# Kernel tuning notes

Measured on AMD Instinct MI355X. Metric: run time of the kernel, lower is better.

The kernel has to match this reference:

```python
import jax, jax.numpy as jnp
import numpy as np

SEQ_LEN = 12      # PRED_LEN
H_DIM = 128
EMB_DIM = 64
NPEDS = 65536


def setup_inputs() -> dict:
    key = jax.random.key(0)
    ks = jax.random.split(key, 12)
    s = 0.05
    return {
        "last_pos": jax.random.normal(ks[0], (NPEDS, 2), jnp.float32),
        "last_pos_rel": jax.random.normal(ks[1], (NPEDS, 2), jnp.float32),
        "h0": jax.random.normal(ks[2], (NPEDS, H_DIM), jnp.float32),
        "c0": jax.random.normal(ks[3], (NPEDS, H_DIM), jnp.float32),
        # LSTM params (torch gate order: i, f, g, o)
        "w_ih": jax.random.normal(ks[4], (4 * H_DIM, EMB_DIM), jnp.float32) * s,
        "w_hh": jax.random.normal(ks[5], (4 * H_DIM, H_DIM), jnp.float32) * s,
        "b_ih": jax.random.normal(ks[6], (4 * H_DIM,), jnp.float32) * s,
        "b_hh": jax.random.normal(ks[7], (4 * H_DIM,), jnp.float32) * s,
        # spatial_embedding: Linear(2, EMB_DIM)
        "w_se": jax.random.normal(ks[8], (EMB_DIM, 2), jnp.float32) * s,
        "b_se": jax.random.normal(ks[9], (EMB_DIM,), jnp.float32) * s,
        # hidden2pos: Linear(H_DIM, 2)
        "w_hp": jax.random.normal(ks[10], (2, H_DIM), jnp.float32) * s,
        "b_hp": jax.random.normal(ks[11], (2,), jnp.float32) * s,
    }


def reference(last_pos, last_pos_rel, h0, c0,
              w_ih, w_hh, b_ih, b_hh, w_se, b_se, w_hp, b_hp):
    b = b_ih + b_hh  # fold the two LSTM biases
    dec_in0 = last_pos_rel @ w_se.T + b_se          # [N, EMB]

    def step(carry, _):
        h, c, dec_in, lp = carry
        gates = dec_in @ w_ih.T + h @ w_hh.T + b    # [N, 4H]
        i, f, g, o = jnp.split(gates, 4, axis=-1)
        c = jax.nn.sigmoid(f) * c + jax.nn.sigmoid(i) * jnp.tanh(g)
        h = jax.nn.sigmoid(o) * jnp.tanh(c)
        rel = h @ w_hp.T + b_hp                     # [N, 2]
        lp = rel + lp                               # curr_pos
        dec_in = rel @ w_se.T + b_se                # next embedding input
        return (h, c, dec_in, lp), rel

    _, rels = jax.lax.scan(step, (h0, c0, dec_in0, last_pos), None, length=SEQ_LEN)
    return rels  # [SEQ_LEN, N, 2] == pred_traj_fake_rel
```

## Files before the change

### kernel.cpp

```cpp
#include <hip/hip_runtime.h>
#include <hip/hip_bf16.h>

typedef __attribute__((ext_vector_type(8))) short bf16x8;
typedef __attribute__((ext_vector_type(4))) short bf16x4;
typedef __attribute__((ext_vector_type(4))) float f32x4;
typedef __attribute__((ext_vector_type(2))) float f32x2;

#define NPEDS 65536
#define SEQ 12
#define HD 128
#define ED 64
#define MBLK 128
#define NPT 8
#define WHH_FRAGS 128
#define WEFF_FRAGS 132
#define NFRAGS (WHH_FRAGS + WEFF_FRAGS)
#define L2E 1.44269504088896340736f
#define NEG2L (-2.88539008177792681472f)

__device__ __forceinline__ short f2bf(float x) {
  __hip_bfloat16 b = __float2bfloat16(x);
  return __builtin_bit_cast(short, b);
}
__device__ __forceinline__ float exp2_(float x) {
#if __has_builtin(__builtin_amdgcn_exp2f)
  return __builtin_amdgcn_exp2f(x);
#else
  return exp2f(x);
#endif
}

__device__ __forceinline__ int hoff(int Pt, int cg, int lhi, int llo) {
  return (((Pt * 8 + cg) * 4 + lhi) * 16 + llo) * 4;
}

__global__ void prep_kernel(const float* __restrict__ w_ih,
                            const float* __restrict__ w_hh,
                            const float* __restrict__ w_se,
                            const float* __restrict__ w_hp,
                            const float* __restrict__ b_ih,
                            const float* __restrict__ b_hh,
                            const float* __restrict__ b_se,
                            const float* __restrict__ b_hp,
                            short* __restrict__ wsB, float* __restrict__ fl) {
  int t = blockIdx.x * 256 + threadIdx.x;
  if (t < WHH_FRAGS * 64) {
    int frag = t >> 6, l = t & 63;
    int cc = frag >> 4, g = (frag >> 2) & 3, kt = frag & 3;
    float fac = (g == 2) ? 2.0f * L2E : L2E;
    int n = g * HD + cc * 16 + (l & 15);
    bf16x8 v;
#pragma unroll
    for (int e = 0; e < 8; ++e) {
      int k = kt * 32 + ((l >> 4) << 2) + (e & 3) + ((e >> 2) << 4);
      v[e] = f2bf(w_hh[n * HD + k] * fac);
    }
    *(bf16x8*)(wsB + (size_t)frag * 512 + l * 8) = v;
  } else if (t < NFRAGS * 64) {
    int u = t - WHH_FRAGS * 64;
    int frag = u >> 6, l = u & 63;
    int llo = l & 15;
    int ks[8];
#pragma unroll
    for (int e = 0; e < 8; ++e)
      ks[e] = (frag & 3) * 32 + ((l >> 4) << 2) + (e & 3) + ((e >> 2) << 4);
    float acc[8];
    if (frag < 128) {
      int cc = frag >> 4, g = (frag >> 2) & 3;
      float fac = (g == 2) ? 2.0f * L2E : L2E;
      int n = g * HD + cc * 16 + llo;
#pragma unroll
      for (int e = 0; e < 8; ++e) acc[e] = w_hh[n * HD + ks[e]];
      for (int j = 0; j < ED; ++j) {
        float wij = w_ih[n * ED + j];
        float se0 = w_se[2 * j], se1 = w_se[2 * j + 1];
#pragma unroll
        for (int e = 0; e < 8; ++e)
          acc[e] += wij * (se0 * w_hp[ks[e]] + se1 * w_hp[HD + ks[e]]);
      }
#pragma unroll
      for (int e = 0; e < 8; ++e) acc[e] *= fac;
    } else {
#pragma unroll
      for (int e = 0; e < 8; ++e)
        acc[e] = (llo < 2) ? w_hp[llo * HD + ks[e]] : 0.f;
    }
    bf16x8 v;
#pragma unroll
    for (int e = 0; e < 8; ++e) v[e] = f2bf(acc[e]);
    *(bf16x8*)(wsB + (size_t)(WHH_FRAGS + frag) * 512 + l * 8) = v;
  } else if (t < NFRAGS * 64 + 512) {
    int n = t - NFRAGS * 64;
    float fac = ((n >> 7) == 2) ? 2.0f * L2E : L2E;
    float b = b_ih[n] + b_hh[n];
    float s0 = 0.f, w20 = 0.f, w21 = 0.f;
    for (int j = 0; j < ED; ++j) {
      float wij = w_ih[n * ED + j];
      s0 += wij * b_se[j];
      w20 += wij * w_se[2 * j];
      w21 += wij * w_se[2 * j + 1];
    }
    fl[n] = fac * (b + s0 + w20 * b_hp[0] + w21 * b_hp[1]);
    fl[512 + n] = fac * (b + s0);
    fl[1024 + 2 * n] = fac * w20;
    fl[1024 + 2 * n + 1] = fac * w21;
  }
}

__global__ __launch_bounds__(512, 2) void lstm_kernel(
    const float* __restrict__ lpr, const float* __restrict__ h0,
    const float* __restrict__ c0, const float* __restrict__ b_hp,
    const short* __restrict__ wsB, const float* __restrict__ fl,
    float* __restrict__ out) {
  __shared__ short hb[2][NPT * 8 * 4 * 16 * 4];

  const int tid = threadIdx.x;
  const int cc = tid >> 6;
  const int l = tid & 63;
  const int lhi = l >> 4;
  const int llo = l & 15;
  const int p0 = blockIdx.x * MBLK;

  bf16x8 Aw[4][4];
#pragma unroll
  for (int g = 0; g < 4; ++g)
#pragma unroll
    for (int kt = 0; kt < 4; ++kt)
      Aw[g][kt] = *(const bf16x8*)(wsB +
                      (size_t)((cc * 4 + g) * 4 + kt) * 512 + l * 8);
  bf16x8 Whp[4];
#pragma unroll
  for (int kt = 0; kt < 4; ++kt)
    Whp[kt] = *(const bf16x8*)(wsB +
                  (size_t)(WHH_FRAGS + 128 + kt) * 512 + l * 8);

  f32x4 beffv[4];
#pragma unroll
  for (int g = 0; g < 4; ++g)
    beffv[g] = *(const f32x4*)&fl[g * HD + cc * 16 + lhi * 4];

  float creg[NPT][4];
#pragma unroll
  for (int Pt = 0; Pt < NPT; ++Pt) {
    f32x4 cv = *(const f32x4*)&c0[(size_t)(p0 + Pt * 16 + llo) * HD +
                                  cc * 16 + lhi * 4];
#pragma unroll
    for (int r = 0; r < 4; ++r) creg[Pt][r] = cv[r];
  }
  const float bhp0 = b_hp[0], bhp1 = b_hp[1];

#pragma unroll
  for (int i = 0; i < 8; ++i) {
    int idx = i * 512 + tid;
    int a = idx & 31, ped = idx >> 5;
    f32x4 v = *(const f32x4*)&h0[(size_t)(p0 + ped) * HD + a * 4];
    bf16x4 sv;
    sv[0] = f2bf(v[0]); sv[1] = f2bf(v[1]);
    sv[2] = f2bf(v[2]); sv[3] = f2bf(v[3]);
    *(bf16x4*)&hb[0][hoff(ped >> 4, a >> 2, a & 3, ped & 15)] = sv;
  }
  __syncthreads();

  auto update_pt = [&](f32x4 (&acc)[4], float (&cr)[4], short* An, int Pt) {
    bf16x4 hn4;
#pragma unroll
    for (int r = 0; r < 4; ++r) {
      float yi = acc[0][r], yf = acc[1][r];
      float yg = acc[2][r], yo = acc[3][r];
      float P = 1.f + exp2_(-yf);
      float Q = 1.f + exp2_(-yi);
      float R = 1.f + exp2_(-yg);
      float QR = Q * R;
      float rD = __builtin_amdgcn_rcpf(P * QR);
      float cn = (cr[r] * QR + (2.f - R) * P) * rD;
      cr[r] = cn;
      float T = 1.f + exp2_(cn * NEG2L);
      float S = 1.f + exp2_(-yo);
      hn4[r] = f2bf((2.f - T) * __builtin_amdgcn_rcpf(S * T));
    }
    *(bf16x4*)&An[hoff(Pt, cc, lhi, llo)] = hn4;
  };

  auto load_bh = [&](bf16x8 (&Bh)[4], const short* A, int Pt) {
#pragma unroll
    for (int kt = 0; kt < 4; ++kt) {
      bf16x4 lo = *(const bf16x4*)&A[hoff(Pt, 2 * kt, lhi, llo)];
      bf16x4 hi = *(const bf16x4*)&A[hoff(Pt, 2 * kt + 1, lhi, llo)];
      Bh[kt] = __builtin_shufflevector(lo, hi, 0, 1, 2, 3, 4, 5, 6, 7);
    }
  };
  auto gates_mfma = [&](f32x4 (&acc)[4], bf16x8 (&Bh)[4]) {
    __builtin_amdgcn_s_setprio(1);
#pragma unroll
    for (int g = 0; g < 4; ++g)
      acc[g] = __builtin_amdgcn_mfma_f32_16x16x32_bf16(Aw[g][0], Bh[0],
                                                       beffv[g], 0, 0, 0);
#pragma unroll
    for (int kt = 1; kt < 4; ++kt)
#pragma unroll
      for (int g = 0; g < 4; ++g)
        acc[g] = __builtin_amdgcn_mfma_f32_16x16x32_bf16(Aw[g][kt], Bh[kt],
                                                         acc[g], 0, 0, 0);
    __builtin_amdgcn_s_setprio(0);
  };
  auto rel_do = [&](bf16x8 (&Bh)[4], int sout) {
    f32x4 ar = {lhi == 0 ? bhp0 : 0.f, lhi == 0 ? bhp1 : 0.f, 0.f, 0.f};
#pragma unroll
    for (int kt = 0; kt < 4; ++kt)
      ar = __builtin_amdgcn_mfma_f32_16x16x32_bf16(Whp[kt], Bh[kt], ar, 0, 0,
                                                   0);
    if (lhi == 0) {
      f32x2 rv = {ar[0], ar[1]};
      *(f32x2*)&out[(size_t)sout * (NPEDS * 2) +
                    (size_t)(p0 + cc * 16 + llo) * 2] = rv;
    }
  };

  {
    f32x4 b0v[4], wa[4], wb[4];
#pragma unroll
    for (int g = 0; g < 4; ++g) {
      int n0 = g * HD + cc * 16 + lhi * 4;
      b0v[g] = *(const f32x4*)&fl[512 + n0];
      wa[g] = *(const f32x4*)&fl[1024 + 2 * n0];
      wb[g] = *(const f32x4*)&fl[1024 + 2 * n0 + 4];
    }
#pragma unroll
    for (int Pt = 0; Pt < NPT; ++Pt) {
      f32x2 lp = *(const f32x2*)&lpr[(size_t)(p0 + Pt * 16 + llo) * 2];
      bf16x8 Bh[4];
      load_bh(Bh, hb[0], Pt);
      f32x4 acc[4];
#pragma unroll
      for (int g = 0; g < 4; ++g) {
        acc[g][0] = b0v[g][0] + wa[g][0] * lp[0] + wa[g][1] * lp[1];
        acc[g][1] = b0v[g][1] + wa[g][2] * lp[0] + wa[g][3] * lp[1];
        acc[g][2] = b0v[g][2] + wb[g][0] * lp[0] + wb[g][1] * lp[1];
        acc[g][3] = b0v[g][3] + wb[g][2] * lp[0] + wb[g][3] * lp[1];
      }
#pragma unroll
      for (int kt = 0; kt < 4; ++kt)
#pragma unroll
        for (int g = 0; g < 4; ++g)
          acc[g] = __builtin_amdgcn_mfma_f32_16x16x32_bf16(Aw[g][kt], Bh[kt],
                                                           acc[g], 0, 0, 0);
      update_pt(acc, creg[Pt], hb[1], Pt);
    }
    __syncthreads();
  }

  const short* wsW = wsB + (size_t)WHH_FRAGS * 512;
#pragma unroll
  for (int g = 0; g < 4; ++g)
#pragma unroll
    for (int kt = 0; kt < 4; ++kt)
      Aw[g][kt] = *(const bf16x8*)(wsW +
                      (size_t)((cc * 4 + g) * 4 + kt) * 512 + l * 8);

  for (int s = 1; s < SEQ; ++s) {
    const short* A = hb[s & 1];
    short* An = hb[(s + 1) & 1];
    bf16x8 BhA[4], BhB[4];
    f32x4 accA[4], accB[4];
    load_bh(BhA, A, 0);
    gates_mfma(accA, BhA);
#pragma unroll
    for (int Pt = 1; Pt < NPT; Pt += 2) {
      load_bh(BhB, A, Pt);
      gates_mfma(accB, BhB);
      if (Pt - 1 == cc) rel_do(BhA, s - 1);
      update_pt(accA, creg[Pt - 1], An, Pt - 1);
      if (Pt + 1 < NPT) {
        load_bh(BhA, A, Pt + 1);
        gates_mfma(accA, BhA);
      }
      if (Pt == cc) rel_do(BhB, s - 1);
      update_pt(accB, creg[Pt], An, Pt);
    }
    __syncthreads();
  }

  {
    bf16x8 Bh[4];
    load_bh(Bh, hb[SEQ & 1], cc);
    rel_do(Bh, SEQ - 1);
  }
}

extern "C" void kernel_launch(void* const* d_in, const int* in_sizes, int n_in,
                              void* d_out, int out_size, void* d_ws,
                              size_t ws_size, hipStream_t stream) {
  const float* lpr = (const float*)d_in[1];
  const float* h0 = (const float*)d_in[2];
  const float* c0 = (const float*)d_in[3];
  const float* w_ih = (const float*)d_in[4];
  const float* w_hh = (const float*)d_in[5];
  const float* b_ih = (const float*)d_in[6];
  const float* b_hh = (const float*)d_in[7];
  const float* w_se = (const float*)d_in[8];
  const float* b_se = (const float*)d_in[9];
  const float* w_hp = (const float*)d_in[10];
  const float* b_hp = (const float*)d_in[11];
  short* wsB = (short*)d_ws;
  float* fl = (float*)((char*)d_ws + (size_t)NFRAGS * 512 * sizeof(short));
  float* out = (float*)d_out;

  prep_kernel<<<67, 256, 0, stream>>>(w_ih, w_hh, w_se, w_hp, b_ih, b_hh,
                                      b_se, b_hp, wsB, fl);
  lstm_kernel<<<NPEDS / MBLK, 512, 0, stream>>>(lpr, h0, c0, b_hp, wsB, fl,
                                                out);
}
```

Baseline: 157.3 us.

## Halve pedestrian tile and move small weights to LDS for higher occupancy

Halves the per-block pedestrian tile from 128 to 64 and raises the launch-bounds target from 2 to 4 blocks per CU. To fit the tighter register budget, it moves the hidden-to-position weights and the gate bias from registers into shared memory, reading them with volatile loads. It also replaces the two-way software-pipelined step loop with a simple sequential loop over tiles. The goal is to hide latency through more resident waves instead of manual interleaving, at the cost of extra LDS traffic and less instruction-level overlap within each wave.

```diff
diff --git a/kernel.cpp b/kernel.cpp
--- a/kernel.cpp
+++ b/kernel.cpp
@@ -10,8 +10,8 @@
 #define SEQ 12
 #define HD 128
 #define ED 64
-#define MBLK 128
-#define NPT 8
+#define MBLK 64
+#define NPT 4
 #define WHH_FRAGS 128
 #define WEFF_FRAGS 132
 #define NFRAGS (WHH_FRAGS + WEFF_FRAGS)
@@ -107,12 +107,14 @@
   }
 }
 
-__global__ __launch_bounds__(512, 2) void lstm_kernel(
+__global__ __launch_bounds__(512, 4) void lstm_kernel(
     const float* __restrict__ lpr, const float* __restrict__ h0,
     const float* __restrict__ c0, const float* __restrict__ b_hp,
     const short* __restrict__ wsB, const float* __restrict__ fl,
     float* __restrict__ out) {
-  __shared__ short hb[2][NPT * 8 * 4 * 16 * 4];
+  __shared__ __align__(16) short hb[2][NPT * 8 * 4 * 16 * 4];
+  __shared__ __align__(16) short s_wsR[4 * 512];
+  __shared__ __align__(16) float s_beff[512];
 
   const int tid = threadIdx.x;
   const int cc = tid >> 6;
@@ -121,6 +123,10 @@
   const int llo = l & 15;
   const int p0 = blockIdx.x * MBLK;
 
+  s_beff[tid] = fl[tid];
+  ((unsigned long long*)s_wsR)[tid] =
+      ((const unsigned long long*)(wsB + (size_t)(WHH_FRAGS + 128) * 512))[tid];
+
   bf16x8 Aw[4][4];
 #pragma unroll
   for (int g = 0; g < 4; ++g)
@@ -128,16 +134,6 @@
     for (int kt = 0; kt < 4; ++kt)
       Aw[g][kt] = *(const bf16x8*)(wsB +
                       (size_t)((cc * 4 + g) * 4 + kt) * 512 + l * 8);
-  bf16x8 Whp[4];
-#pragma unroll
-  for (int kt = 0; kt < 4; ++kt)
-    Whp[kt] = *(const bf16x8*)(wsB +
-                  (size_t)(WHH_FRAGS + 128 + kt) * 512 + l * 8);
-
-  f32x4 beffv[4];
-#pragma unroll
-  for (int g = 0; g < 4; ++g)
-    beffv[g] = *(const f32x4*)&fl[g * HD + cc * 16 + lhi * 4];
 
   float creg[NPT][4];
 #pragma unroll
@@ -150,7 +146,7 @@
   const float bhp0 = b_hp[0], bhp1 = b_hp[1];
 
 #pragma unroll
-  for (int i = 0; i < 8; ++i) {
+  for (int i = 0; i < 4; ++i) {
     int idx = i * 512 + tid;
     int a = idx & 31, ped = idx >> 5;
     f32x4 v = *(const f32x4*)&h0[(size_t)(p0 + ped) * HD + a * 4];
@@ -192,9 +188,11 @@
   auto gates_mfma = [&](f32x4 (&acc)[4], bf16x8 (&Bh)[4]) {
     __builtin_amdgcn_s_setprio(1);
 #pragma unroll
-    for (int g = 0; g < 4; ++g)
-      acc[g] = __builtin_amdgcn_mfma_f32_16x16x32_bf16(Aw[g][0], Bh[0],
-                                                       beffv[g], 0, 0, 0);
+    for (int g = 0; g < 4; ++g) {
+      f32x4 c4 = *(volatile const f32x4*)&s_beff[g * HD + cc * 16 + lhi * 4];
+      acc[g] = __builtin_amdgcn_mfma_f32_16x16x32_bf16(Aw[g][0], Bh[0], c4, 0,
+                                                       0, 0);
+    }
 #pragma unroll
     for (int kt = 1; kt < 4; ++kt)
 #pragma unroll
@@ -206,9 +204,10 @@
   auto rel_do = [&](bf16x8 (&Bh)[4], int sout) {
     f32x4 ar = {lhi == 0 ? bhp0 : 0.f, lhi == 0 ? bhp1 : 0.f, 0.f, 0.f};
 #pragma unroll
-    for (int kt = 0; kt < 4; ++kt)
-      ar = __builtin_amdgcn_mfma_f32_16x16x32_bf16(Whp[kt], Bh[kt], ar, 0, 0,
-                                                   0);
+    for (int kt = 0; kt < 4; ++kt) {
+      bf16x8 wt = *(volatile const bf16x8*)(s_wsR + kt * 512 + l * 8);
+      ar = __builtin_amdgcn_mfma_f32_16x16x32_bf16(wt, Bh[kt], ar, 0, 0, 0);
+    }
     if (lhi == 0) {
       f32x2 rv = {ar[0], ar[1]};
       *(f32x2*)&out[(size_t)sout * (NPEDS * 2) +
@@ -217,33 +216,30 @@
   };
 
   {
-    f32x4 b0v[4], wa[4], wb[4];
-#pragma unroll
-    for (int g = 0; g < 4; ++g) {
-      int n0 = g * HD + cc * 16 + lhi * 4;
-      b0v[g] = *(const f32x4*)&fl[512 + n0];
-      wa[g] = *(const f32x4*)&fl[1024 + 2 * n0];
-      wb[g] = *(const f32x4*)&fl[1024 + 2 * n0 + 4];
-    }
+    bf16x8 Bh[4];
+    f32x4 acc[4];
 #pragma unroll
     for (int Pt = 0; Pt < NPT; ++Pt) {
+      load_bh(Bh, hb[0], Pt);
       f32x2 lp = *(const f32x2*)&lpr[(size_t)(p0 + Pt * 16 + llo) * 2];
-      bf16x8 Bh[4];
-      load_bh(Bh, hb[0], Pt);
-      f32x4 acc[4];
 #pragma unroll
       for (int g = 0; g < 4; ++g) {
-        acc[g][0] = b0v[g][0] + wa[g][0] * lp[0] + wa[g][1] * lp[1];
-        acc[g][1] = b0v[g][1] + wa[g][2] * lp[0] + wa[g][3] * lp[1];
-        acc[g][2] = b0v[g][2] + wb[g][0] * lp[0] + wb[g][1] * lp[1];
-        acc[g][3] = b0v[g][3] + wb[g][2] * lp[0] + wb[g][3] * lp[1];
-      }
-#pragma unroll
-      for (int kt = 0; kt < 4; ++kt)
-#pragma unroll
-        for (int g = 0; g < 4; ++g)
+        int n0 = g * HD + cc * 16 + lhi * 4;
+        f32x4 b0 = *(const f32x4*)&fl[512 + n0];
+        f32x4 wa = *(const f32x4*)&fl[1024 + 2 * n0];
+        f32x4 wb = *(const f32x4*)&fl[1024 + 2 * n0 + 4];
+        f32x4 ci;
+        ci[0] = b0[0] + wa[0] * lp[0] + wa[1] * lp[1];
+        ci[1] = b0[1] + wa[2] * lp[0] + wa[3] * lp[1];
+        ci[2] = b0[2] + wb[0] * lp[0] + wb[1] * lp[1];
+        ci[3] = b0[3] + wb[2] * lp[0] + wb[3] * lp[1];
+        acc[g] = __builtin_amdgcn_mfma_f32_16x16x32_bf16(Aw[g][0], Bh[0], ci,
+                                                         0, 0, 0);
+#pragma unroll
+        for (int kt = 1; kt < 4; ++kt)
           acc[g] = __builtin_amdgcn_mfma_f32_16x16x32_bf16(Aw[g][kt], Bh[kt],
                                                            acc[g], 0, 0, 0);
+      }
       update_pt(acc, creg[Pt], hb[1], Pt);
     }
     __syncthreads();
@@ -260,27 +256,19 @@
   for (int s = 1; s < SEQ; ++s) {
     const short* A = hb[s & 1];
     short* An = hb[(s + 1) & 1];
-    bf16x8 BhA[4], BhB[4];
-    f32x4 accA[4], accB[4];
-    load_bh(BhA, A, 0);
-    gates_mfma(accA, BhA);
-#pragma unroll
-    for (int Pt = 1; Pt < NPT; Pt += 2) {
-      load_bh(BhB, A, Pt);
-      gates_mfma(accB, BhB);
-      if (Pt - 1 == cc) rel_do(BhA, s - 1);
-      update_pt(accA, creg[Pt - 1], An, Pt - 1);
-      if (Pt + 1 < NPT) {
-        load_bh(BhA, A, Pt + 1);
-        gates_mfma(accA, BhA);
-      }
-      if (Pt == cc) rel_do(BhB, s - 1);
-      update_pt(accB, creg[Pt], An, Pt);
+    bf16x8 Bh[4];
+    f32x4 acc[4];
+#pragma unroll
+    for (int Pt = 0; Pt < NPT; ++Pt) {
+      load_bh(Bh, A, Pt);
+      gates_mfma(acc, Bh);
+      if (Pt == cc) rel_do(Bh, s - 1);
+      update_pt(acc, creg[Pt], An, Pt);
     }
     __syncthreads();
   }
 
-  {
+  if (cc < NPT) {
     bf16x8 Bh[4];
     load_bh(Bh, hb[SEQ & 1], cc);
     rel_do(Bh, SEQ - 1);
```

Result: slower. 289.1 us (+83.8%).
